# Kernel optimization log

Measured on AMD Instinct MI355X. Metric: run time of the kernel, lower is better.

## Reference

```python
import jax, jax.numpy as jnp
import numpy as np
import math

EMBED_DIM = 256
NUM_HEADS = 8
NUM_LEVELS = 4
NUM_POINTS = 4
HEAD_DIM = EMBED_DIM // NUM_HEADS
SPATIAL_SHAPES = np.array([[100, 100], [50, 50], [25, 25], [13, 13]], dtype=np.int64)
LEN_V = int((SPATIAL_SHAPES[:, 0] * SPATIAL_SHAPES[:, 1]).sum())  # 13294
BS, LEN_Q = 8, 1024


def _grid_sample_bilinear(img, grid):
    """img: [N, C, H, W]; grid: [N, Hg, Wg, 2] in [-1,1].
    bilinear, padding_mode='zeros', align_corners=False. Returns [N, Hg, Wg, C]."""
    N, C, H, W = img.shape
    x = (grid[..., 0] + 1.0) * (W * 0.5) - 0.5
    y = (grid[..., 1] + 1.0) * (H * 0.5) - 0.5
    x0 = jnp.floor(x)
    y0 = jnp.floor(y)
    x1 = x0 + 1.0
    y1 = y0 + 1.0
    wx1 = x - x0
    wx0 = 1.0 - wx1
    wy1 = y - y0
    wy0 = 1.0 - wy1
    b = jnp.arange(N)[:, None, None]

    def gather(yi, xi):
        valid = (yi >= 0) & (yi <= H - 1) & (xi >= 0) & (xi <= W - 1)
        yc = jnp.clip(yi, 0, H - 1).astype(jnp.int32)
        xc = jnp.clip(xi, 0, W - 1).astype(jnp.int32)
        v = img[b, :, yc, xc]  # [N, Hg, Wg, C]
        return v * valid[..., None].astype(img.dtype)

    out = (gather(y0, x0) * (wy0 * wx0)[..., None]
           + gather(y0, x1) * (wy0 * wx1)[..., None]
           + gather(y1, x0) * (wy1 * wx0)[..., None]
           + gather(y1, x1) * (wy1 * wx1)[..., None])
    return out


def _offset_bias_init():
    # Faithful to _reset_parameters: per-head directional grid init for offsets bias.
    thetas = np.arange(NUM_HEADS, dtype=np.float32) * (2.0 * math.pi / NUM_HEADS)
    g = np.stack([np.cos(thetas), np.sin(thetas)], -1)
    g = g / np.abs(g).max(-1, keepdims=True)
    g = np.tile(g.reshape(NUM_HEADS, 1, 1, 2), (1, NUM_LEVELS, NUM_POINTS, 1))
    g = g * np.arange(1, NUM_POINTS + 1, dtype=np.float32).reshape(1, 1, -1, 1)
    return jnp.asarray(g.reshape(-1))


def setup_inputs() -> dict:
    key = jax.random.key(0)
    ks = jax.random.split(key, 8)
    TP = NUM_HEADS * NUM_LEVELS * NUM_POINTS  # 128

    def xavier(k, fan_in, fan_out):
        lim = math.sqrt(6.0 / (fan_in + fan_out))
        return jax.random.uniform(k, (fan_in, fan_out), jnp.float32, -lim, lim)

    return {
        "query": jax.random.normal(ks[0], (BS, LEN_Q, EMBED_DIM), jnp.float32),
        "reference_points": jax.random.uniform(ks[1], (BS, LEN_Q, NUM_LEVELS, 2), jnp.float32),
        "value": jax.random.normal(ks[2], (BS, LEN_V, EMBED_DIM), jnp.float32),
        "value_spatial_shapes": SPATIAL_SHAPES,
        # small random weights (instead of the zero-init) so the math paths are exercised
        "so_w": 0.01 * jax.random.normal(ks[3], (EMBED_DIM, TP * 2), jnp.float32),
        "so_b": _offset_bias_init(),
        "aw_w": 0.01 * jax.random.normal(ks[4], (EMBED_DIM, TP), jnp.float32),
        "aw_b": jnp.zeros((TP,), jnp.float32),
        "vp_w": xavier(ks[5], EMBED_DIM, EMBED_DIM),
        "vp_b": jnp.zeros((EMBED_DIM,), jnp.float32),
        "op_w": xavier(ks[6], EMBED_DIM, EMBED_DIM),
        "op_b": jnp.zeros((EMBED_DIM,), jnp.float32),
    }


def reference(query, reference_points, value, value_spatial_shapes,
              so_w, so_b, aw_w, aw_b, vp_w, vp_b, op_w, op_b):
    shapes = np.asarray(value_spatial_shapes)  # static python ints
    bs, len_q, D = query.shape
    H, L, P, hd = NUM_HEADS, NUM_LEVELS, NUM_POINTS, HEAD_DIM

    v = value @ vp_w + vp_b                              # [bs, len_v, D]
    v = v.reshape(bs, -1, H, hd)                         # [bs, len_v, H, hd]

    so = (query @ so_w + so_b).reshape(bs, len_q, H, L, P, 2)
    aw = (query @ aw_w + aw_b).reshape(bs, len_q, H, L * P)
    aw = jax.nn.softmax(aw, axis=-1).reshape(bs, len_q, H, L, P)

    # reference_points last dim == 2 branch: normalize offsets by (w, h) per level
    norm = jnp.asarray(shapes[:, ::-1].copy(), dtype=query.dtype).reshape(1, 1, 1, L, 1, 2)
    loc = reference_points.reshape(bs, len_q, 1, L, 1, 2) + so / norm
    grids = 2.0 * loc - 1.0                              # [bs, len_q, H, L, P, 2]
    grids = grids.transpose(0, 2, 1, 3, 4, 5).reshape(bs * H, len_q, L, P, 2)

    samples = []
    start = 0
    for lvl in range(L):
        h, w = int(shapes[lvl, 0]), int(shapes[lvl, 1])
        vl = v[:, start:start + h * w]                   # [bs, hw, H, hd]
        start += h * w
        img = vl.transpose(0, 2, 3, 1).reshape(bs * H, hd, h, w)
        s = _grid_sample_bilinear(img, grids[:, :, lvl])  # [bs*H, len_q, P, hd]
        samples.append(s)
    samp = jnp.stack(samples, axis=2)                    # [bs*H, len_q, L, P, hd]

    w_ = aw.transpose(0, 2, 1, 3, 4).reshape(bs * H, len_q, L, P)
    out = jnp.einsum('nqlpd,nqlp->nqd', samp, w_)        # [bs*H, len_q, hd]
    out = out.reshape(bs, H, len_q, hd).transpose(0, 2, 1, 3).reshape(bs, len_q, D)
    return out @ op_w + op_b
```

## Files before the change

kernel.cpp:

```cpp
#include <hip/hip_runtime.h>
#include <hip/hip_bf16.h>
#include <math.h>

#define BSZ 8
#define LQ  1024
#define LV  13294
#define NH  8
#define HD  32
#define VM  (BSZ * LV)
#define MQ  (BSZ * LQ)
#define NVB ((VM + 63) / 64)

typedef __attribute__((ext_vector_type(8))) short bf16x8;
typedef __attribute__((ext_vector_type(4))) float f32x4;

__device__ static inline unsigned short f2bf(float f) {
    unsigned int u = __float_as_uint(f);
    unsigned int r = (u + 0x7FFFu + ((u >> 16) & 1u)) >> 16;
    return (unsigned short)r;
}
__device__ static inline float bf2f(unsigned short s) {
    return __uint_as_float(((unsigned int)s) << 16);
}
__device__ static inline unsigned int pk2bf(float a, float b) {
    __hip_bfloat162 h = __float22bfloat162_rn(make_float2(a, b));
    return *(unsigned int*)&h;
}

__global__ __launch_bounds__(256) void prep_kernel(
    const float* __restrict__ vp_w, const float* __restrict__ op_w,
    const float* __restrict__ so_w, const float* __restrict__ aw_w,
    unsigned short* __restrict__ wTv, unsigned short* __restrict__ wTo,
    unsigned short* __restrict__ wTso, unsigned short* __restrict__ wTaw)
{
    const int blk = blockIdx.x;
    const int t   = threadIdx.x;
    if (blk < 768) {
        const int n = blk & 255;
        const int k = t;
        const float* w; unsigned short* o;
        if      (blk < 256) { w = vp_w; o = wTv; }
        else if (blk < 512) { w = op_w; o = wTo; }
        else                { w = so_w; o = wTso; }
        o[(((k >> 5) * 256 + n) << 5) + (k & 31)] = f2bf(w[k * 256 + n]);
    } else {
        const int n = blk - 768;
        const int k = t;
        wTaw[(((k >> 5) * 128 + n) << 5) + (k & 31)] = f2bf(aw_w[k * 128 + n]);
    }
}

template<int NJ>
__device__ __forceinline__ void gemm16_split_body(
    unsigned short* __restrict__ lds,
    const float* __restrict__ Q,
    const unsigned short* __restrict__ wT, const float* __restrict__ bias,
    float* __restrict__ C, int m0)
{
    constexpr int N = NJ * 64;
    unsigned short* Ah = lds;
    unsigned short* Al = lds + 16 * 256;

    const int tid  = threadIdx.x;
    const int w    = tid >> 6;
    const int lane = tid & 63;
    const int mrow = lane & 15;
    const int quad = lane >> 4;

#pragma unroll
    for (int r = 0; r < 2; ++r) {
        const int flat = r * 256 + tid;
        const int row  = flat >> 5;
        const int ck   = flat & 31;
        const float* qp = Q + (size_t)(m0 + row) * 256 + ck * 8;
        const float4 f0 = *(const float4*)qp;
        const float4 f1 = *(const float4*)(qp + 4);
        ushort4 h0, l0v;
        h0.x = f2bf(f0.x); l0v.x = f2bf(f0.x - bf2f(h0.x));
        h0.y = f2bf(f0.y); l0v.y = f2bf(f0.y - bf2f(h0.y));
        h0.z = f2bf(f0.z); l0v.z = f2bf(f0.z - bf2f(h0.z));
        h0.w = f2bf(f0.w); l0v.w = f2bf(f0.w - bf2f(h0.w));
        ushort4 h1, l1v;
        h1.x = f2bf(f1.x); l1v.x = f2bf(f1.x - bf2f(h1.x));
        h1.y = f2bf(f1.y); l1v.y = f2bf(f1.y - bf2f(h1.y));
        h1.z = f2bf(f1.z); l1v.z = f2bf(f1.z - bf2f(h1.z));
        h1.w = f2bf(f1.w); l1v.w = f2bf(f1.w - bf2f(h1.w));
        const int cp = ck ^ row;
        *(ushort4*)&Ah[row * 256 + cp * 8]     = h0;
        *(ushort4*)&Ah[row * 256 + cp * 8 + 4] = h1;
        *(ushort4*)&Al[row * 256 + cp * 8]     = l0v;
        *(ushort4*)&Al[row * 256 + cp * 8 + 4] = l1v;
    }
    __syncthreads();

    f32x4 acc[NJ];
#pragma unroll
    for (int j = 0; j < NJ; ++j) acc[j] = (f32x4)0.f;

#pragma unroll
    for (int kc = 0; kc < 8; ++kc) {
        bf16x8 wf[NJ];
#pragma unroll
        for (int j = 0; j < NJ; ++j) {
            const int n = w * (NJ * 16) + j * 16 + mrow;
            wf[j] = *(const bf16x8*)(const void*)(wT + (((size_t)kc * N + n) << 5) + quad * 8);
        }
        const int cp = (kc * 4 + quad) ^ mrow;
        const bf16x8 af  = *(const bf16x8*)(const void*)&Ah[mrow * 256 + cp * 8];
        const bf16x8 af2 = *(const bf16x8*)(const void*)&Al[mrow * 256 + cp * 8];
#pragma unroll
        for (int j = 0; j < NJ; ++j)
            acc[j] = __builtin_amdgcn_mfma_f32_16x16x32_bf16(wf[j], af, acc[j], 0, 0, 0);
#pragma unroll
        for (int j = 0; j < NJ; ++j)
            acc[j] = __builtin_amdgcn_mfma_f32_16x16x32_bf16(wf[j], af2, acc[j], 0, 0, 0);
    }

    const int gm = m0 + mrow;
#pragma unroll
    for (int j = 0; j < NJ; ++j) {
        const int col = w * (NJ * 16) + j * 16 + quad * 4;
        const float4 bb = *(const float4*)(bias + col);
        float4 o;
        o.x = acc[j][0] + bb.x;
        o.y = acc[j][1] + bb.y;
        o.z = acc[j][2] + bb.z;
        o.w = acc[j][3] + bb.w;
        *(float4*)(C + (size_t)gm * N + col) = o;
    }
}

__device__ __forceinline__ void gemm16_bf16_body(
    unsigned short* __restrict__ lds,
    const unsigned short* __restrict__ A,
    const unsigned short* __restrict__ wT, const float* __restrict__ bias,
    float* __restrict__ C, int m0)
{
    unsigned short* Ah = lds;
    const int tid  = threadIdx.x;
    const int w    = tid >> 6;
    const int lane = tid & 63;
    const int mrow = lane & 15;
    const int quad = lane >> 4;

#pragma unroll
    for (int r = 0; r < 2; ++r) {
        const int flat = r * 256 + tid;
        const int row  = flat >> 5;
        const int ck   = flat & 31;
        const int cp   = ck ^ row;
        *(uint4*)&Ah[row * 256 + cp * 8] =
            *(const uint4*)(A + (size_t)(m0 + row) * 256 + ck * 8);
    }
    __syncthreads();

    f32x4 acc[4];
#pragma unroll
    for (int j = 0; j < 4; ++j) acc[j] = (f32x4)0.f;

#pragma unroll
    for (int kc = 0; kc < 8; ++kc) {
        bf16x8 wf[4];
#pragma unroll
        for (int j = 0; j < 4; ++j) {
            const int n = w * 64 + j * 16 + mrow;
            wf[j] = *(const bf16x8*)(const void*)(wT + (((size_t)kc * 256 + n) << 5) + quad * 8);
        }
        const int cp = (kc * 4 + quad) ^ mrow;
        const bf16x8 af = *(const bf16x8*)(const void*)&Ah[mrow * 256 + cp * 8];
#pragma unroll
        for (int j = 0; j < 4; ++j)
            acc[j] = __builtin_amdgcn_mfma_f32_16x16x32_bf16(wf[j], af, acc[j], 0, 0, 0);
    }

    const int gm = m0 + mrow;
#pragma unroll
    for (int j = 0; j < 4; ++j) {
        const int col = w * 64 + j * 16 + quad * 4;
        const float4 bb = *(const float4*)(bias + col);
        float4 o;
        o.x = acc[j][0] + bb.x;
        o.y = acc[j][1] + bb.y;
        o.z = acc[j][2] + bb.z;
        o.w = acc[j][3] + bb.w;
        *(float4*)(C + (size_t)gm * 256 + col) = o;
    }
}

__global__ __launch_bounds__(256, 4) void fused1_kernel(
    const float* __restrict__ A,
    const unsigned short* __restrict__ wTv,
    const float* __restrict__ vp_b,
    unsigned short* __restrict__ v,
    const float* __restrict__ query,
    const unsigned short* __restrict__ wTso, const float* __restrict__ so_b,
    float* __restrict__ so_raw,
    const unsigned short* __restrict__ wTaw, const float* __restrict__ aw_b,
    float* __restrict__ aw_raw)
{
    __shared__ __align__(16) unsigned short lds_u16[64 * 256];

    const int blk = blockIdx.x;
    if (blk >= NVB) {
        if (blk < NVB + 512)
            gemm16_split_body<4>(lds_u16, query, wTso, so_b, so_raw,
                                 (blk - NVB) * 16);
        else
            gemm16_split_body<2>(lds_u16, query, wTaw, aw_b, aw_raw,
                                 (blk - NVB - 512) * 16);
        return;
    }

    const int tid  = threadIdx.x;
    const int w    = tid >> 6;
    const int lane = tid & 63;
    const int mrow = lane & 15;
    const int quad = lane >> 4;
    const int m0   = blk * 64;

#pragma unroll
    for (int r = 0; r < 16; ++r) {
        const int flat = r * 256 + tid;
        const int grow = flat >> 6;
        const int gcol = flat & 63;
        int gm = m0 + grow; if (gm >= VM) gm = VM - 1;
        const float4 f = *(const float4*)(A + (size_t)gm * 256 + gcol * 4);
        uint2 pk;
        pk.x = pk2bf(f.x, f.y);
        pk.y = pk2bf(f.z, f.w);
        const int c  = gcol >> 1;
        const int cp = c ^ (grow & 31);
        *(uint2*)&lds_u16[grow * 256 + cp * 8 + (gcol & 1) * 4] = pk;
    }
    __syncthreads();

    f32x4 acc[4][4];
#pragma unroll
    for (int i = 0; i < 4; ++i)
#pragma unroll
        for (int j = 0; j < 4; ++j) acc[i][j] = (f32x4)0.f;

#define LOADW(dst, kc_) {                                                     \
        _Pragma("unroll")                                                     \
        for (int j = 0; j < 4; ++j) {                                         \
            const int n = w * 64 + j * 16 + mrow;                             \
            dst[j] = *(const bf16x8*)(const void*)(wTv +                      \
                       (((size_t)(kc_) * 256 + n) << 5) + quad * 8);          \
        }                                                                     \
    }

    bf16x8 wcur[4], wnext[4];
    LOADW(wcur, 0);
    LOADW(wnext, 1);

#pragma unroll
    for (int kc = 0; kc < 8; ++kc) {
        bf16x8 af[4];
#pragma unroll
        for (int i = 0; i < 4; ++i) {
            const int mr = i * 16 + mrow;
            const int cp = (kc * 4 + quad) ^ (mr & 31);
            af[i] = *(const bf16x8*)(const void*)&lds_u16[mr * 256 + cp * 8];
        }
#pragma unroll
        for (int i = 0; i < 4; ++i)
#pragma unroll
            for (int j = 0; j < 4; ++j)
                acc[i][j] = __builtin_amdgcn_mfma_f32_16x16x32_bf16(
                    wcur[j], af[i], acc[i][j], 0, 0, 0);
#pragma unroll
        for (int j = 0; j < 4; ++j) wcur[j] = wnext[j];
        if (kc < 6) LOADW(wnext, kc + 2);
    }
#undef LOADW

    float4 bj[4];
#pragma unroll
    for (int j = 0; j < 4; ++j)
        bj[j] = *(const float4*)(vp_b + w * 64 + j * 16 + quad * 4);

#pragma unroll
    for (int i = 0; i < 4; ++i) {
        const int gm = m0 + i * 16 + mrow;
        if (gm >= VM) continue;
        const unsigned int b   = (unsigned int)gm / (unsigned int)LV;
        const unsigned int pix = (unsigned int)gm - b * (unsigned int)LV;
#pragma unroll
        for (int j = 0; j < 4; ++j) {
            const int ch = w * 64 + j * 16 + quad * 4;
            const int h  = ch >> 5, cc = ch & 31;
            uint2 o;
            o.x = pk2bf(acc[i][j][0] + bj[j].x, acc[i][j][1] + bj[j].y);
            o.y = pk2bf(acc[i][j][2] + bj[j].z, acc[i][j][3] + bj[j].w);
            *(uint2*)(v + (((size_t)(b * NH + h)) * LV + pix) * HD + cc) = o;
        }
    }
}

__global__ __launch_bounds__(256) void oproj_kernel(
    const unsigned short* __restrict__ Ah,
    const unsigned short* __restrict__ wTo,
    const float* __restrict__ bias,
    float* __restrict__ C)
{
    __shared__ __align__(16) unsigned short lds_u16[16 * 256];
    gemm16_bf16_body(lds_u16, Ah, wTo, bias, C, blockIdx.x * 16);
}

__global__ __launch_bounds__(256) void sample_kernel(
    const unsigned short* __restrict__ v,
    const float* __restrict__ so_raw,
    const float* __restrict__ aw_raw,
    const float* __restrict__ refp,
    unsigned short* __restrict__ out_head)
{
    const int blk = blockIdx.x;
    const int bh  = blk >> 8;
    const int j2  = blk & 255;
    const int b   = bh >> 3;
    const int h   = bh & 7;

    const int wv   = threadIdx.x >> 6;
    const int lane = threadIdx.x & 63;
    const int ch   = lane & 7;
    const int pz   = lane >> 3;

    const int q  = j2 * 4 + wv;
    const int rq = b * LQ + q;

    const float l0 = aw_raw[rq * 128 + h * 16 + pz];
    const float l1 = aw_raw[rq * 128 + h * 16 + 8 + pz];
    float mx = fmaxf(l0, l1);
    mx = fmaxf(mx, __shfl_xor(mx, 8));
    mx = fmaxf(mx, __shfl_xor(mx, 16));
    mx = fmaxf(mx, __shfl_xor(mx, 32));
    const float e0 = __expf(l0 - mx), e1 = __expf(l1 - mx);
    float sm = e0 + e1;
    sm += __shfl_xor(sm, 8);
    sm += __shfl_xor(sm, 16);
    sm += __shfl_xor(sm, 32);
    const float inv_s = 1.f / sm;

    const unsigned short* vb = v + (size_t)bh * (LV * HD) + ch * 4;

    float a0 = 0.f, a1 = 0.f, a2 = 0.f, a3 = 0.f;

#pragma unroll
    for (int r = 0; r < 2; ++r) {
        const int pt = r * 8 + pz;
        const int l  = pt >> 2;
        const int p  = pt & 3;
        const float wgt = (r ? e1 : e0) * inv_s;

        const int Wl = (l == 0) ? 100 : (l == 1) ? 50 : (l == 2) ? 25 : 13;
        const int st = (l == 0) ? 0 : (l == 1) ? 10000 : (l == 2) ? 12500 : 13125;
        const float invW = (l == 0) ? 0.01f : (l == 1) ? 0.02f : (l == 2) ? 0.04f
                                            : (1.0f / 13.0f);
        const float fw = (float)Wl;

        const float2 rxy = *(const float2*)(refp + (size_t)rq * 8 + l * 2);
        const float2 sxy = *(const float2*)(so_raw + (size_t)rq * 256 + h * 32 + l * 8 + p * 2);

        const float x = (rxy.x + sxy.x * invW) * fw - 0.5f;
        const float y = (rxy.y + sxy.y * invW) * fw - 0.5f;

        const float xf = floorf(x), yf = floorf(y);
        const int x0 = (int)xf, y0 = (int)yf;
        const float wx1 = x - xf, wx0 = 1.f - wx1;
        const float wy1 = y - yf, wy0 = 1.f - wy1;

        const float vx0 = (x0 >= 0 && x0 < Wl) ? 1.f : 0.f;
        const float vx1 = (x0 + 1 >= 0 && x0 + 1 < Wl) ? 1.f : 0.f;
        const float vy0 = (y0 >= 0 && y0 < Wl) ? 1.f : 0.f;
        const float vy1 = (y0 + 1 >= 0 && y0 + 1 < Wl) ? 1.f : 0.f;

        const int xc0 = min(max(x0, 0), Wl - 1);
        const int xc1 = min(max(x0 + 1, 0), Wl - 1);
        const int yc0 = min(max(y0, 0), Wl - 1);
        const int yc1 = min(max(y0 + 1, 0), Wl - 1);

        const float w00 = wgt * wy0 * wx0 * vy0 * vx0;
        const float w01 = wgt * wy0 * wx1 * vy0 * vx1;
        const float w10 = wgt * wy1 * wx0 * vy1 * vx0;
        const float w11 = wgt * wy1 * wx1 * vy1 * vx1;

        const int row0 = (st + yc0 * Wl) * HD;
        const int row1 = (st + yc1 * Wl) * HD;

        const ushort4 u00 = *(const ushort4*)(vb + row0 + xc0 * HD);
        const ushort4 u01 = *(const ushort4*)(vb + row0 + xc1 * HD);
        const ushort4 u10 = *(const ushort4*)(vb + row1 + xc0 * HD);
        const ushort4 u11 = *(const ushort4*)(vb + row1 + xc1 * HD);

        a0 = fmaf(w00, bf2f(u00.x), a0);
        a1 = fmaf(w00, bf2f(u00.y), a1);
        a2 = fmaf(w00, bf2f(u00.z), a2);
        a3 = fmaf(w00, bf2f(u00.w), a3);
        a0 = fmaf(w01, bf2f(u01.x), a0);
        a1 = fmaf(w01, bf2f(u01.y), a1);
        a2 = fmaf(w01, bf2f(u01.z), a2);
        a3 = fmaf(w01, bf2f(u01.w), a3);
        a0 = fmaf(w10, bf2f(u10.x), a0);
        a1 = fmaf(w10, bf2f(u10.y), a1);
        a2 = fmaf(w10, bf2f(u10.z), a2);
        a3 = fmaf(w10, bf2f(u10.w), a3);
        a0 = fmaf(w11, bf2f(u11.x), a0);
        a1 = fmaf(w11, bf2f(u11.y), a1);
        a2 = fmaf(w11, bf2f(u11.z), a2);
        a3 = fmaf(w11, bf2f(u11.w), a3);
    }

    a0 += __shfl_xor(a0, 8);  a1 += __shfl_xor(a1, 8);
    a2 += __shfl_xor(a2, 8);  a3 += __shfl_xor(a3, 8);
    a0 += __shfl_xor(a0, 16); a1 += __shfl_xor(a1, 16);
    a2 += __shfl_xor(a2, 16); a3 += __shfl_xor(a3, 16);
    a0 += __shfl_xor(a0, 32); a1 += __shfl_xor(a1, 32);
    a2 += __shfl_xor(a2, 32); a3 += __shfl_xor(a3, 32);

    if (pz == 0) {
        uint2 o;
        o.x = pk2bf(a0, a1);
        o.y = pk2bf(a2, a3);
        *(uint2*)(out_head + (size_t)rq * 256 + (h << 5) + (ch << 2)) = o;
    }
}

extern "C" void kernel_launch(void* const* d_in, const int* in_sizes, int n_in,
                              void* d_out, int out_size, void* d_ws, size_t ws_size,
                              hipStream_t stream)
{
    const float* query = (const float*)d_in[0];
    const float* refp  = (const float*)d_in[1];
    const float* value = (const float*)d_in[2];
    const float* so_w  = (const float*)d_in[4];
    const float* so_b  = (const float*)d_in[5];
    const float* aw_w  = (const float*)d_in[6];
    const float* aw_b  = (const float*)d_in[7];
    const float* vp_w  = (const float*)d_in[8];
    const float* vp_b  = (const float*)d_in[9];
    const float* op_w  = (const float*)d_in[10];
    const float* op_b  = (const float*)d_in[11];
    float* out = (float*)d_out;

    float* ws = (float*)d_ws;
    size_t off = 0;
    unsigned short* v = (unsigned short*)(ws + off);
    off += (size_t)BSZ * NH * LV * HD / 2;
    unsigned short* wTv  = (unsigned short*)(ws + off); off += 32768;
    unsigned short* wTo  = (unsigned short*)(ws + off); off += 32768;
    unsigned short* wTso = (unsigned short*)(ws + off); off += 32768;
    unsigned short* wTaw = (unsigned short*)(ws + off); off += 16384;
    float* so_raw = ws + off; off += (size_t)MQ * 256;
    float* aw_raw = ws + off; off += (size_t)MQ * 128;
    unsigned short* out_head = (unsigned short*)(ws + off);
    off += (size_t)MQ * 128;

    prep_kernel<<<896, 256, 0, stream>>>(vp_w, op_w, so_w, aw_w,
                                         wTv, wTo, wTso, wTaw);

    fused1_kernel<<<NVB + 1024, 256, 0, stream>>>(
        value, wTv, vp_b, v, query, wTso, so_b, so_raw, wTaw, aw_b, aw_raw);

    sample_kernel<<<BSZ * NH * LQ / 4, 256, 0, stream>>>(
        v, so_raw, aw_raw, refp, out_head);

    oproj_kernel<<<MQ / 16, 256, 0, stream>>>(out_head, wTo, op_b, out);
}
```

Measured before the change: 247.2 us.

## Widen GEMM blocks to 512 threads with per-wave head column split

Moves the value-projection, query-projection and output-projection GEMMs to 512-thread blocks. Each of the eight waves now owns 32 output columns, which is one head, so the value-store epilogue writes one contiguous per-head row. The query GEMMs handle two 16-row tiles per block, and the output projection now processes 64 rows per block with the A tile staged in shared memory. This lowers per-block launch and weight-fetch overhead and improves locality of the stores. In exchange it drops the weight-fragment double-buffering prefetch and raises register and LDS pressure per block.

```diff
diff --git a/kernel.cpp b/kernel.cpp
--- a/kernel.cpp
+++ b/kernel.cpp
@@ -55,21 +55,25 @@
     unsigned short* __restrict__ lds,
     const float* __restrict__ Q,
     const unsigned short* __restrict__ wT, const float* __restrict__ bias,
-    float* __restrict__ C, int m0)
+    float* __restrict__ C, int m0_blk)
 {
     constexpr int N = NJ * 64;
-    unsigned short* Ah = lds;
-    unsigned short* Al = lds + 16 * 256;
-
     const int tid  = threadIdx.x;
-    const int w    = tid >> 6;
+    const int w8   = tid >> 6;
+    const int half = w8 >> 2;
+    const int w    = w8 & 3;
     const int lane = tid & 63;
     const int mrow = lane & 15;
     const int quad = lane >> 4;
-
+    const int m0   = m0_blk + half * 16;
+
+    unsigned short* Ah = lds + half * 8192;
+    unsigned short* Al = Ah + 16 * 256;
+
+    const int ht = tid & 255;
 #pragma unroll
     for (int r = 0; r < 2; ++r) {
-        const int flat = r * 256 + tid;
+        const int flat = r * 256 + ht;
         const int row  = flat >> 5;
         const int ck   = flat & 31;
         const float* qp = Q + (size_t)(m0 + row) * 256 + ck * 8;
@@ -130,64 +134,7 @@
     }
 }
 
-__device__ __forceinline__ void gemm16_bf16_body(
-    unsigned short* __restrict__ lds,
-    const unsigned short* __restrict__ A,
-    const unsigned short* __restrict__ wT, const float* __restrict__ bias,
-    float* __restrict__ C, int m0)
-{
-    unsigned short* Ah = lds;
-    const int tid  = threadIdx.x;
-    const int w    = tid >> 6;
-    const int lane = tid & 63;
-    const int mrow = lane & 15;
-    const int quad = lane >> 4;
-
-#pragma unroll
-    for (int r = 0; r < 2; ++r) {
-        const int flat = r * 256 + tid;
-        const int row  = flat >> 5;
-        const int ck   = flat & 31;
-        const int cp   = ck ^ row;
-        *(uint4*)&Ah[row * 256 + cp * 8] =
-            *(const uint4*)(A + (size_t)(m0 + row) * 256 + ck * 8);
-    }
-    __syncthreads();
-
-    f32x4 acc[4];
-#pragma unroll
-    for (int j = 0; j < 4; ++j) acc[j] = (f32x4)0.f;
-
-#pragma unroll
-    for (int kc = 0; kc < 8; ++kc) {
-        bf16x8 wf[4];
-#pragma unroll
-        for (int j = 0; j < 4; ++j) {
-            const int n = w * 64 + j * 16 + mrow;
-            wf[j] = *(const bf16x8*)(const void*)(wT + (((size_t)kc * 256 + n) << 5) + quad * 8);
-        }
-        const int cp = (kc * 4 + quad) ^ mrow;
-        const bf16x8 af = *(const bf16x8*)(const void*)&Ah[mrow * 256 + cp * 8];
-#pragma unroll
-        for (int j = 0; j < 4; ++j)
-            acc[j] = __builtin_amdgcn_mfma_f32_16x16x32_bf16(wf[j], af, acc[j], 0, 0, 0);
-    }
-
-    const int gm = m0 + mrow;
-#pragma unroll
-    for (int j = 0; j < 4; ++j) {
-        const int col = w * 64 + j * 16 + quad * 4;
-        const float4 bb = *(const float4*)(bias + col);
-        float4 o;
-        o.x = acc[j][0] + bb.x;
-        o.y = acc[j][1] + bb.y;
-        o.z = acc[j][2] + bb.z;
-        o.w = acc[j][3] + bb.w;
-        *(float4*)(C + (size_t)gm * 256 + col) = o;
-    }
-}
-
-__global__ __launch_bounds__(256, 4) void fused1_kernel(
+__global__ __launch_bounds__(512, 4) void fused1_kernel(
     const float* __restrict__ A,
     const unsigned short* __restrict__ wTv,
     const float* __restrict__ vp_b,
@@ -202,12 +149,12 @@
 
     const int blk = blockIdx.x;
     if (blk >= NVB) {
-        if (blk < NVB + 512)
+        if (blk < NVB + 256)
             gemm16_split_body<4>(lds_u16, query, wTso, so_b, so_raw,
-                                 (blk - NVB) * 16);
+                                 (blk - NVB) * 32);
         else
             gemm16_split_body<2>(lds_u16, query, wTaw, aw_b, aw_raw,
-                                 (blk - NVB - 512) * 16);
+                                 (blk - NVB - 256) * 32);
         return;
     }
 
@@ -219,8 +166,8 @@
     const int m0   = blk * 64;
 
 #pragma unroll
-    for (int r = 0; r < 16; ++r) {
-        const int flat = r * 256 + tid;
+    for (int r = 0; r < 8; ++r) {
+        const int flat = r * 512 + tid;
         const int grow = flat >> 6;
         const int gcol = flat & 63;
         int gm = m0 + grow; if (gm >= VM) gm = VM - 1;
@@ -234,28 +181,20 @@
     }
     __syncthreads();
 
-    f32x4 acc[4][4];
+    f32x4 acc[4][2];
 #pragma unroll
     for (int i = 0; i < 4; ++i)
 #pragma unroll
-        for (int j = 0; j < 4; ++j) acc[i][j] = (f32x4)0.f;
-
-#define LOADW(dst, kc_) {                                                     \
-        _Pragma("unroll")                                                     \
-        for (int j = 0; j < 4; ++j) {                                         \
-            const int n = w * 64 + j * 16 + mrow;                             \
-            dst[j] = *(const bf16x8*)(const void*)(wTv +                      \
-                       (((size_t)(kc_) * 256 + n) << 5) + quad * 8);          \
-        }                                                                     \
-    }
-
-    bf16x8 wcur[4], wnext[4];
-    LOADW(wcur, 0);
-    LOADW(wnext, 1);
+        for (int j = 0; j < 2; ++j) acc[i][j] = (f32x4)0.f;
 
 #pragma unroll
     for (int kc = 0; kc < 8; ++kc) {
-        bf16x8 af[4];
+        bf16x8 wfr[2], af[4];
+#pragma unroll
+        for (int j = 0; j < 2; ++j) {
+            const int n = w * 32 + j * 16 + mrow;
+            wfr[j] = *(const bf16x8*)(const void*)(wTv + (((size_t)kc * 256 + n) << 5) + quad * 8);
+        }
 #pragma unroll
         for (int i = 0; i < 4; ++i) {
             const int mr = i * 16 + mrow;
@@ -265,19 +204,15 @@
 #pragma unroll
         for (int i = 0; i < 4; ++i)
 #pragma unroll
-            for (int j = 0; j < 4; ++j)
+            for (int j = 0; j < 2; ++j)
                 acc[i][j] = __builtin_amdgcn_mfma_f32_16x16x32_bf16(
-                    wcur[j], af[i], acc[i][j], 0, 0, 0);
-#pragma unroll
-        for (int j = 0; j < 4; ++j) wcur[j] = wnext[j];
-        if (kc < 6) LOADW(wnext, kc + 2);
-    }
-#undef LOADW
-
-    float4 bj[4];
-#pragma unroll
-    for (int j = 0; j < 4; ++j)
-        bj[j] = *(const float4*)(vp_b + w * 64 + j * 16 + quad * 4);
+                    wfr[j], af[i], acc[i][j], 0, 0, 0);
+    }
+
+    float4 bj[2];
+#pragma unroll
+    for (int j = 0; j < 2; ++j)
+        bj[j] = *(const float4*)(vp_b + w * 32 + j * 16 + quad * 4);
 
 #pragma unroll
     for (int i = 0; i < 4; ++i) {
@@ -285,26 +220,89 @@
         if (gm >= VM) continue;
         const unsigned int b   = (unsigned int)gm / (unsigned int)LV;
         const unsigned int pix = (unsigned int)gm - b * (unsigned int)LV;
-#pragma unroll
-        for (int j = 0; j < 4; ++j) {
-            const int ch = w * 64 + j * 16 + quad * 4;
-            const int h  = ch >> 5, cc = ch & 31;
+        unsigned short* vp = v + (((size_t)(b * NH + w)) * LV + pix) * HD;
+#pragma unroll
+        for (int j = 0; j < 2; ++j) {
             uint2 o;
             o.x = pk2bf(acc[i][j][0] + bj[j].x, acc[i][j][1] + bj[j].y);
             o.y = pk2bf(acc[i][j][2] + bj[j].z, acc[i][j][3] + bj[j].w);
-            *(uint2*)(v + (((size_t)(b * NH + h)) * LV + pix) * HD + cc) = o;
-        }
-    }
-}
-
-__global__ __launch_bounds__(256) void oproj_kernel(
+            *(uint2*)(vp + j * 16 + quad * 4) = o;
+        }
+    }
+}
+
+__global__ __launch_bounds__(512, 4) void oproj_kernel(
     const unsigned short* __restrict__ Ah,
     const unsigned short* __restrict__ wTo,
     const float* __restrict__ bias,
-    float* __restrict__ C)
-{
-    __shared__ __align__(16) unsigned short lds_u16[16 * 256];
-    gemm16_bf16_body(lds_u16, Ah, wTo, bias, C, blockIdx.x * 16);
+    float* __restrict__ out)
+{
+    __shared__ __align__(16) unsigned short lds_u16[64 * 256];
+
+    const int tid  = threadIdx.x;
+    const int w    = tid >> 6;
+    const int lane = tid & 63;
+    const int mrow = lane & 15;
+    const int quad = lane >> 4;
+    const int m0   = blockIdx.x * 64;
+
+#pragma unroll
+    for (int r = 0; r < 4; ++r) {
+        const int flat = r * 512 + tid;
+        const int row  = flat >> 5;
+        const int ck   = flat & 31;
+        const int cp   = ck ^ (row & 31);
+        *(uint4*)&lds_u16[row * 256 + cp * 8] =
+            *(const uint4*)(Ah + (size_t)(m0 + row) * 256 + ck * 8);
+    }
+    __syncthreads();
+
+    f32x4 acc[4][2];
+#pragma unroll
+    for (int i = 0; i < 4; ++i)
+#pragma unroll
+        for (int j = 0; j < 2; ++j) acc[i][j] = (f32x4)0.f;
+
+#pragma unroll
+    for (int kc = 0; kc < 8; ++kc) {
+        bf16x8 wfr[2], af[4];
+#pragma unroll
+        for (int j = 0; j < 2; ++j) {
+            const int n = w * 32 + j * 16 + mrow;
+            wfr[j] = *(const bf16x8*)(const void*)(wTo + (((size_t)kc * 256 + n) << 5) + quad * 8);
+        }
+#pragma unroll
+        for (int i = 0; i < 4; ++i) {
+            const int mr = i * 16 + mrow;
+            const int cp = (kc * 4 + quad) ^ (mr & 31);
+            af[i] = *(const bf16x8*)(const void*)&lds_u16[mr * 256 + cp * 8];
+        }
+#pragma unroll
+        for (int i = 0; i < 4; ++i)
+#pragma unroll
+            for (int j = 0; j < 2; ++j)
+                acc[i][j] = __builtin_amdgcn_mfma_f32_16x16x32_bf16(
+                    wfr[j], af[i], acc[i][j], 0, 0, 0);
+    }
+
+    float4 bj[2];
+#pragma unroll
+    for (int j = 0; j < 2; ++j)
+        bj[j] = *(const float4*)(bias + w * 32 + j * 16 + quad * 4);
+
+#pragma unroll
+    for (int i = 0; i < 4; ++i) {
+        const int gm = m0 + i * 16 + mrow;
+#pragma unroll
+        for (int j = 0; j < 2; ++j) {
+            float4 o;
+            o.x = acc[i][j][0] + bj[j].x;
+            o.y = acc[i][j][1] + bj[j].y;
+            o.z = acc[i][j][2] + bj[j].z;
+            o.w = acc[i][j][3] + bj[j].w;
+            *(float4*)(out + (size_t)gm * 256 + w * 32 + j * 16 + quad * 4) = o;
+        }
+    }
 }
 
 __global__ __launch_bounds__(256) void sample_kernel(
@@ -458,11 +456,11 @@
     prep_kernel<<<896, 256, 0, stream>>>(vp_w, op_w, so_w, aw_w,
                                          wTv, wTo, wTso, wTaw);
 
-    fused1_kernel<<<NVB + 1024, 256, 0, stream>>>(
+    fused1_kernel<<<NVB + 512, 512, 0, stream>>>(
         value, wTv, vp_b, v, query, wTso, so_b, so_raw, wTaw, aw_b, aw_raw);
 
     sample_kernel<<<BSZ * NH * LQ / 4, 256, 0, stream>>>(
         v, so_raw, aw_raw, refp, out_head);
 
-    oproj_kernel<<<MQ / 16, 256, 0, stream>>>(out_head, wTo, op_b, out);
-}
+    oproj_kernel<<<MQ / 64, 512, 0, stream>>>(out_head, wTo, op_b, out);
+}
```

Result: no change. 247.1 us (-0.0%).
